# Kernel tuning notes

Measured on AMD Instinct MI355X. Metric: run time of the kernel, lower is better.

## Reference

```python
import jax, jax.numpy as jnp
import numpy as np

B, H, W, C, G = 4, 64, 64, 512, 32
EPS = 1e-5


def group_norm(x, gamma, beta):
    b, h, w, c = x.shape
    xg = x.reshape(b, h, w, G, c // G)
    mean = xg.mean(axis=(1, 2, 4), keepdims=True)
    var = xg.var(axis=(1, 2, 4), keepdims=True)
    xn = ((xg - mean) * jax.lax.rsqrt(var + EPS)).reshape(b, h, w, c)
    return xn * gamma + beta


def setup_inputs() -> dict:
    key = jax.random.key(0)
    ks = jax.random.split(key, 6)
    s = 0.02  # conv-weight init scale
    return {
        "x": jax.random.normal(ks[0], (B, H, W, C), jnp.float32),
        "gamma": jnp.ones((C,), jnp.float32),
        "beta": jnp.zeros((C,), jnp.float32),
        "Wq": jax.random.normal(ks[1], (C, C), jnp.float32) * s,
        "bq": jnp.zeros((C,), jnp.float32),
        "Wk": jax.random.normal(ks[2], (C, C), jnp.float32) * s,
        "bk": jnp.zeros((C,), jnp.float32),
        "Wv": jax.random.normal(ks[3], (C, C), jnp.float32) * s,
        "bv": jnp.zeros((C,), jnp.float32),
        "Wp": jax.random.normal(ks[4], (C, C), jnp.float32) * s,
        "bp": jnp.zeros((C,), jnp.float32),
    }


def reference(x, gamma, beta, Wq, bq, Wk, bk, Wv, bv, Wp, bp):
    b, h, w, c = x.shape
    xn = group_norm(x, gamma, beta)
    # 1x1 convs == per-pixel linear
    q = (jnp.einsum('bhwc,cd->bhwd', xn, Wq) + bq).reshape(b, h * w, c)
    k = (jnp.einsum('bhwc,cd->bhwd', xn, Wk) + bk).reshape(b, h * w, c)
    v = (jnp.einsum('bhwc,cd->bhwd', xn, Wv) + bv).reshape(b, h * w, c)
    scale = 1.0 / jnp.sqrt(jnp.asarray(c, x.dtype))
    scores = jnp.einsum('bqc,bkc->bqk', q, k) * scale  # [b, hw, hw]
    attn = jax.nn.softmax(scores, axis=-1)
    out = jnp.einsum('bqk,bkc->bqc', attn, v).reshape(b, h, w, c)
    return jnp.einsum('bhwc,cd->bhwd', out, Wp) + bp + x
```

## Files before the change

kernel.cpp:

```cpp
#include <hip/hip_runtime.h>

typedef unsigned short u16;
typedef unsigned char u8;
typedef short bf16x8 __attribute__((ext_vector_type(8)));
typedef float f32x4 __attribute__((ext_vector_type(4)));
typedef int i32x8 __attribute__((ext_vector_type(8)));

#define CH 512
#define HW 4096
#define TOKENS 16384
#define NGRP 32

__device__ __forceinline__ u16 f2bf(float f) {
  unsigned u = __float_as_uint(f);
  u += 0x7fffu + ((u >> 16) & 1u);
  return (u16)(u >> 16);
}
__device__ __forceinline__ u8 f2fp8(float f) {
  return (u8)(__builtin_amdgcn_cvt_pk_fp8_f32(f, f, 0, false) & 0xff);
}
__device__ __forceinline__ unsigned f2fp8x4(float a, float b, float c, float d) {
  int lo = __builtin_amdgcn_cvt_pk_fp8_f32(a, b, 0, false);
  return (unsigned)__builtin_amdgcn_cvt_pk_fp8_f32(c, d, lo, true);
}

#define GLOAD16(gp, lp)                                                        \
  __builtin_amdgcn_global_load_lds(                                            \
      (const __attribute__((address_space(1))) unsigned int*)(const void*)(gp),\
      (__attribute__((address_space(3))) unsigned int*)(void*)(lp), 16, 0, 0)

#define RD_FRAG(dst, buf, row) do {                                            \
    int base_ = (row) * 128, sw_ = ((row) & 7) << 4;                           \
    uint4 lo_ = *(const uint4*)(&buf[base_ + ((h * 32) ^ sw_)]);               \
    uint4 hi_ = *(const uint4*)(&buf[base_ + ((h * 32 + 16) ^ sw_)]);          \
    dst[0] = (int)lo_.x; dst[1] = (int)lo_.y; dst[2] = (int)lo_.z;             \
    dst[3] = (int)lo_.w; dst[4] = (int)hi_.x; dst[5] = (int)hi_.y;             \
    dst[6] = (int)hi_.z; dst[7] = (int)hi_.w;                                  \
  } while (0)

#define MXMFMA(a, b, c) \
  __builtin_amdgcn_mfma_scale_f32_16x16x128_f8f6f4(a, b, c, 0, 0, 0, 127, 0, 127)

__global__ void gn_stats(const float* __restrict__ x, float2* __restrict__ stats) {
  int bg = blockIdx.x;
  int b = bg >> 5, g = bg & 31;
  const float* base = x + (size_t)b * HW * CH + g * 16;
  float s = 0.f, s2 = 0.f;
  for (int p = threadIdx.x; p < HW; p += 256) {
    const float4* row = (const float4*)(base + (size_t)p * CH);
#pragma unroll
    for (int q = 0; q < 4; ++q) {
      float4 v = row[q];
      s += v.x + v.y + v.z + v.w;
      s2 += v.x * v.x + v.y * v.y + v.z * v.z + v.w * v.w;
    }
  }
#pragma unroll
  for (int o = 32; o; o >>= 1) { s += __shfl_down(s, o); s2 += __shfl_down(s2, o); }
  __shared__ float rs[4], rs2[4];
  int wid = threadIdx.x >> 6, lane = threadIdx.x & 63;
  if (lane == 0) { rs[wid] = s; rs2[wid] = s2; }
  __syncthreads();
  if (threadIdx.x == 0) {
    float S = rs[0] + rs[1] + rs[2] + rs[3];
    float S2 = rs2[0] + rs2[1] + rs2[2] + rs2[3];
    float mean = S * (1.f / 65536.f);
    float var = S2 * (1.f / 65536.f) - mean * mean;
    stats[bg] = make_float2(mean, rsqrtf(var + 1e-5f));
  }
}

__global__ void gn_apply8(const float* __restrict__ x, const float* __restrict__ gamma,
                          const float* __restrict__ beta, const float2* __restrict__ stats,
                          u8* __restrict__ xn8) {
  size_t i = (size_t)blockIdx.x * blockDim.x + threadIdx.x;
  size_t e0 = i * 8;
  int c = (int)(e0 & (CH - 1));
  size_t t = e0 >> 9;
  int b = (int)(t >> 12);
  float2 st = stats[b * NGRP + (c >> 4)];
  float4 v0 = *(const float4*)(x + t * CH + c);
  float4 v1 = *(const float4*)(x + t * CH + c + 4);
  float4 g0 = *(const float4*)(gamma + c);
  float4 g1 = *(const float4*)(gamma + c + 4);
  float4 b0 = *(const float4*)(beta + c);
  float4 b1 = *(const float4*)(beta + c + 4);
  float o[8];
  o[0] = (v0.x - st.x) * st.y * g0.x + b0.x;
  o[1] = (v0.y - st.x) * st.y * g0.y + b0.y;
  o[2] = (v0.z - st.x) * st.y * g0.z + b0.z;
  o[3] = (v0.w - st.x) * st.y * g0.w + b0.w;
  o[4] = (v1.x - st.x) * st.y * g1.x + b1.x;
  o[5] = (v1.y - st.x) * st.y * g1.y + b1.y;
  o[6] = (v1.z - st.x) * st.y * g1.z + b1.z;
  o[7] = (v1.w - st.x) * st.y * g1.w + b1.w;
  uint2 pk;
  pk.x = f2fp8x4(o[0], o[1], o[2], o[3]);
  pk.y = f2fp8x4(o[4], o[5], o[6], o[7]);
  *(uint2*)(xn8 + e0) = pk;
}

__global__ void transpose_w8(const float* __restrict__ W0, const float* __restrict__ W1,
                             const float* __restrict__ W2, const float* __restrict__ W3,
                             u8* __restrict__ T0, u8* __restrict__ T1,
                             u8* __restrict__ T2, u8* __restrict__ T3) {
  const float* W; u8* T;
  switch (blockIdx.z) {
    case 0: W = W0; T = T0; break;
    case 1: W = W1; T = T1; break;
    case 2: W = W2; T = T2; break;
    default: W = W3; T = T3; break;
  }
  __shared__ float tile[32][33];
  int tx = threadIdx.x, ty = threadIdx.y;
  int x0 = blockIdx.x * 32, y0 = blockIdx.y * 32;
#pragma unroll
  for (int r = 0; r < 32; r += 8) tile[ty + r][tx] = W[(size_t)(y0 + ty + r) * CH + x0 + tx];
  __syncthreads();
#pragma unroll
  for (int r = 0; r < 32; r += 8) T[(size_t)(x0 + ty + r) * CH + y0 + tx] = f2fp8(tile[tx][ty + r]);
}

template <int MODE>
__global__ __launch_bounds__(256) void gemm8mx(const u8* __restrict__ A,
                                               const u8* __restrict__ Bt,
                                               const float* __restrict__ b0p,
                                               const float* __restrict__ b1p,
                                               const float* __restrict__ b2p,
                                               const float* __restrict__ residual,
                                               const float* __restrict__ lsum_in,
                                               float* __restrict__ lsum_out,
                                               void* __restrict__ Cout,
                                               void* __restrict__ C2,
                                               void* __restrict__ C3,
                                               int N, int K, float scale,
                                               size_t sA, size_t sB, size_t sC) {
  constexpr int BK = 128;
  __shared__ __align__(16) u8 lA[128 * BK];
  __shared__ __align__(16) u8 lB[128 * BK];
  __shared__ float lsum_sh[(MODE == 4) ? 128 : 1];

  int bm, bn, z;
  if constexpr (MODE == 4) {
    if (gridDim.y == 1) {
      int p = blockIdx.x;
      int xcd = p & 7, j = p >> 3;
      int xi = j & 3;
      int mp = xcd * 16 + (j >> 2);
      bn = xi * 128; bm = (mp & 31) * 128; z = mp >> 5;
    } else {
      z = blockIdx.z; bm = blockIdx.y * 128; bn = blockIdx.x * 128;
    }
  } else {
    z = blockIdx.z; bm = blockIdx.y * 128; bn = blockIdx.x * 128;
  }
  A += (size_t)z * sA;
  Bt += (size_t)z * sB;

  const int tid = threadIdx.x, lane = tid & 63, wid = tid >> 6;
  const int wm = (wid >> 1) * 64, wn = (wid & 1) * 64;
  const int r0 = lane & 15, h = lane >> 4;

  if constexpr (MODE == 4) {
    if (tid < 128) {
      const float* lp = lsum_in + (size_t)(z * 64) * HW + bm + tid;
      float s = 0.f;
#pragma unroll 8
      for (int p = 0; p < 64; ++p) s += lp[(size_t)p * HW];
      lsum_sh[tid] = s;
    }
  }

  const int srow = lane >> 3;
  const int scol = ((lane & 7) * 16) ^ ((srow & 7) << 4);
  size_t aoff[4], boff[4];
#pragma unroll
  for (int s = 0; s < 4; ++s) {
    int row = wid * 32 + s * 8 + srow;
    aoff[s] = (size_t)(bm + row) * K + scol;
    boff[s] = (size_t)(bn + row) * K + scol;
  }

  f32x4 acc[4][4] = {};

  for (int kt = 0; kt < K; kt += BK) {
    __syncthreads();
#pragma unroll
    for (int s = 0; s < 4; ++s) {
      GLOAD16(A + aoff[s] + kt, &lA[(wid * 4 + s) * 1024]);
      GLOAD16(Bt + boff[s] + kt, &lB[(wid * 4 + s) * 1024]);
    }
    __syncthreads();
    i32x8 bf[4];
#pragma unroll
    for (int j = 0; j < 4; ++j) RD_FRAG(bf[j], lB, wn + j * 16 + r0);
#pragma unroll
    for (int i = 0; i < 4; ++i) {
      i32x8 af;
      RD_FRAG(af, lA, wm + i * 16 + r0);
#pragma unroll
      for (int j = 0; j < 4; ++j) acc[i][j] = MXMFMA(af, bf[j], acc[i][j]);
    }
  }

  if constexpr (MODE == 5) {
    u8* C = (u8*)Cout + (size_t)z * sC;
    float* lp = lsum_out + (size_t)(z * 64 + blockIdx.x * 2 + (wid & 1)) * HW;
#pragma unroll
    for (int i = 0; i < 4; ++i) {
      int m0 = bm + wm + i * 16 + h * 4;
      float rs[4] = {0.f, 0.f, 0.f, 0.f};
#pragma unroll
      for (int j = 0; j < 4; ++j) {
        int n = bn + wn + j * 16 + r0;
#pragma unroll
        for (int r = 0; r < 4; ++r) {
          float e = __expf(acc[i][j][r] * scale);
          rs[r] += e;
          C[(size_t)(m0 + r) * N + n] = f2fp8(e);
        }
      }
#pragma unroll
      for (int r = 0; r < 4; ++r) {
#pragma unroll
        for (int w = 1; w < 16; w <<= 1) rs[r] += __shfl_xor(rs[r], w);
        if (r0 == 0) lp[m0 + r] = rs[r];
      }
    }
  } else {
#pragma unroll
    for (int j = 0; j < 4; ++j) {
      int n = bn + wn + j * 16 + r0;
#pragma unroll
      for (int i = 0; i < 4; ++i) {
        int m0 = bm + wm + i * 16 + h * 4;
        if constexpr (MODE == 2) {
          float* C = (float*)Cout;
          float bvv = b0p[n];
#pragma unroll
          for (int r = 0; r < 4; ++r) {
            size_t idx = (size_t)(m0 + r) * N + n;
            C[idx] = acc[i][j][r] + bvv + residual[idx];
          }
        } else if constexpr (MODE == 3) {
          int nn = n & 511, ch = n >> 9;
          float bvv = ch == 0 ? b0p[nn] : ch == 1 ? b1p[nn] : b2p[nn];
          float v[4];
#pragma unroll
          for (int r = 0; r < 4; ++r) v[r] = acc[i][j][r] + bvv;
          if (ch == 2) {
            int bb = m0 >> 12, tl = m0 & (HW - 1);
            *(unsigned*)((u8*)C3 + ((size_t)bb * CH + nn) * HW + tl) =
                f2fp8x4(v[0], v[1], v[2], v[3]);
          } else {
            u8* C = (u8*)(ch == 0 ? Cout : C2);
#pragma unroll
            for (int r = 0; r < 4; ++r) C[(size_t)(m0 + r) * CH + nn] = f2fp8(v[r]);
          }
        } else {
          u8* C = (u8*)Cout + (size_t)z * sC;
#pragma unroll
          for (int r = 0; r < 4; ++r) {
            float inv = 1.0f / lsum_sh[wm + i * 16 + h * 4 + r];
            C[(size_t)(m0 + r) * N + n] = f2fp8(acc[i][j][r] * inv);
          }
        }
      }
    }
  }
}

__global__ __launch_bounds__(256) void sgemm8(const u8* __restrict__ A,
                                              const u8* __restrict__ Bt,
                                              float* __restrict__ lsum,
                                              u8* __restrict__ S8,
                                              int M, int N, int K, float scale,
                                              size_t sA, size_t sB, size_t sC) {
  constexpr int BM = 128, BN = 128, BK = 64, LRB = 80;
  __shared__ __align__(16) u8 lA[BM * LRB];
  __shared__ __align__(16) u8 lB[BN * LRB];
  const int z = blockIdx.z;
  A += (size_t)z * sA;
  Bt += (size_t)z * sB;
  const int tid = threadIdx.x;
  const int lane = tid & 63, wid = tid >> 6;
  const int bm = blockIdx.y * BM, bn = blockIdx.x * BN;
  const int wm = (wid >> 1) * 64, wn = (wid & 1) * 64;
  const int r0 = lane & 15, h = lane >> 4;

  f32x4 acc[4][4] = {};
  for (int kt = 0; kt < K; kt += BK) {
    __syncthreads();
#pragma unroll
    for (int s = 0; s < 2; ++s) {
      int cid = tid + s * 256;
      int row = cid >> 2, col = (cid & 3) * 16;
      *(uint4*)(&lA[row * LRB + col]) =
          *(const uint4*)(A + (size_t)(bm + row) * K + kt + col);
      *(uint4*)(&lB[row * LRB + col]) =
          *(const uint4*)(Bt + (size_t)(bn + row) * K + kt + col);
    }
    __syncthreads();
#pragma unroll
    for (int kk = 0; kk < BK; kk += 32) {
      long af[4], bfr[4];
#pragma unroll
      for (int i = 0; i < 4; ++i)
        af[i] = *(const long*)(&lA[(wm + i * 16 + r0) * LRB + kk + h * 8]);
#pragma unroll
      for (int j = 0; j < 4; ++j)
        bfr[j] = *(const long*)(&lB[(wn + j * 16 + r0) * LRB + kk + h * 8]);
#pragma unroll
      for (int i = 0; i < 4; ++i)
#pragma unroll
        for (int j = 0; j < 4; ++j)
          acc[i][j] = __builtin_amdgcn_mfma_f32_16x16x32_fp8_fp8(af[i], bfr[j], acc[i][j], 0, 0, 0);
    }
  }

  u8* C = S8 + (size_t)z * sC;
  float* lp = lsum + (size_t)(z * 64 + blockIdx.x * 2 + (wid & 1)) * HW;
#pragma unroll
  for (int i = 0; i < 4; ++i) {
    int m0 = bm + wm + i * 16 + h * 4;
    float rs[4] = {0.f, 0.f, 0.f, 0.f};
#pragma unroll
    for (int j = 0; j < 4; ++j) {
      int n = bn + wn + j * 16 + r0;
#pragma unroll
      for (int r = 0; r < 4; ++r) {
        float e = __expf(acc[i][j][r] * scale);
        rs[r] += e;
        C[(size_t)(m0 + r) * N + n] = f2fp8(e);
      }
    }
#pragma unroll
    for (int r = 0; r < 4; ++r) {
#pragma unroll
      for (int w = 1; w < 16; w <<= 1) rs[r] += __shfl_xor(rs[r], w);
      if (r0 == 0) lp[m0 + r] = rs[r];
    }
  }
}

__global__ __launch_bounds__(256) void pv8(const u8* __restrict__ A,
                                           const u8* __restrict__ Bt,
                                           const float* __restrict__ lsum,
                                           u8* __restrict__ Ob8,
                                           int M, int N, int K,
                                           size_t sA, size_t sB, size_t sC) {
  constexpr int BM = 128, BN = 128, BK = 64, LRB = 80;
  __shared__ __align__(16) u8 lA[BM * LRB];
  __shared__ __align__(16) u8 lB[BN * LRB];
  __shared__ float lsum_sh[BM];

  int bm, bn, z;
  z = blockIdx.z; bm = blockIdx.y * BM; bn = blockIdx.x * BN;
  A += (size_t)z * sA;
  Bt += (size_t)z * sB;
  const int tid = threadIdx.x;
  const int lane = tid & 63, wid = tid >> 6;
  const int wm = (wid >> 1) * 64, wn = (wid & 1) * 64;
  const int r0 = lane & 15, h = lane >> 4;

  if (tid < BM) {
    const float* lp = lsum + (size_t)(z * 64) * HW + bm + tid;
    float s = 0.f;
#pragma unroll 8
    for (int p = 0; p < 64; ++p) s += lp[(size_t)p * HW];
    lsum_sh[tid] = s;
  }

  f32x4 acc[4][4] = {};
  for (int kt = 0; kt < K; kt += BK) {
    __syncthreads();
#pragma unroll
    for (int s = 0; s < 2; ++s) {
      int cid = tid + s * 256;
      int row = cid >> 2, col = (cid & 3) * 16;
      *(uint4*)(&lA[row * LRB + col]) =
          *(const uint4*)(A + (size_t)(bm + row) * K + kt + col);
      *(uint4*)(&lB[row * LRB + col]) =
          *(const uint4*)(Bt + (size_t)(bn + row) * K + kt + col);
    }
    __syncthreads();
#pragma unroll
    for (int kk = 0; kk < BK; kk += 32) {
      long af[4], bfr[4];
#pragma unroll
      for (int i = 0; i < 4; ++i)
        af[i] = *(const long*)(&lA[(wm + i * 16 + r0) * LRB + kk + h * 8]);
#pragma unroll
      for (int j = 0; j < 4; ++j)
        bfr[j] = *(const long*)(&lB[(wn + j * 16 + r0) * LRB + kk + h * 8]);
#pragma unroll
      for (int i = 0; i < 4; ++i)
#pragma unroll
        for (int j = 0; j < 4; ++j)
          acc[i][j] = __builtin_amdgcn_mfma_f32_16x16x32_fp8_fp8(af[i], bfr[j], acc[i][j], 0, 0, 0);
    }
  }

  u8* C = Ob8 + (size_t)z * sC;
#pragma unroll
  for (int j = 0; j < 4; ++j) {
    int n = bn + wn + j * 16 + r0;
#pragma unroll
    for (int i = 0; i < 4; ++i) {
      int m0 = bm + wm + i * 16 + h * 4;
#pragma unroll
      for (int r = 0; r < 4; ++r) {
        float inv = 1.0f / lsum_sh[wm + i * 16 + h * 4 + r];
        C[(size_t)(m0 + r) * N + n] = f2fp8(acc[i][j][r] * inv);
      }
    }
  }
}

extern "C" void kernel_launch(void* const* d_in, const int* in_sizes, int n_in,
                              void* d_out, int out_size, void* d_ws, size_t ws_size,
                              hipStream_t stream) {
  (void)in_sizes; (void)n_in; (void)out_size;
  const float* x     = (const float*)d_in[0];
  const float* gamma = (const float*)d_in[1];
  const float* beta  = (const float*)d_in[2];
  const float* Wq    = (const float*)d_in[3];
  const float* bq    = (const float*)d_in[4];
  const float* Wk    = (const float*)d_in[5];
  const float* bk    = (const float*)d_in[6];
  const float* Wv    = (const float*)d_in[7];
  const float* bv    = (const float*)d_in[8];
  const float* Wp    = (const float*)d_in[9];
  const float* bp    = (const float*)d_in[10];
  float* out = (float*)d_out;

  char* ws = (char*)d_ws;
  size_t off = 0;
  auto alloc = [&](size_t bytes) -> void* {
    void* p = ws + off;
    off += (bytes + 255) & ~(size_t)255;
    return p;
  };
  const size_t X8  = (size_t)TOKENS * CH;
  const size_t W8  = (size_t)CH * CH;
  const size_t S8B = (size_t)HW * HW;
  const size_t LS  = (size_t)4 * 64 * HW * sizeof(float);
  const size_t need_all = 1024 * 1024 + LS + 5 * X8 + 4 * W8 + 4 * S8B;
  const bool big = ws_size >= need_all;

  float2* stats    = (float2*)alloc(128 * sizeof(float2));
  float* lsum_part = (float*)alloc(LS);
  u8* xn8   = (u8*)alloc(X8);
  u8* O8    = (u8*)alloc(X8);
  u8* Q8    = (u8*)alloc(X8);
  u8* K8    = (u8*)alloc(X8);
  u8* V8t   = (u8*)alloc(X8);
  u8* Wqkv8 = (u8*)alloc(3 * W8);
  u8* Wp8   = (u8*)alloc(W8);
  u8* S8    = (u8*)alloc(big ? 4 * S8B : S8B);

  gn_stats<<<128, 256, 0, stream>>>(x, stats);
  gn_apply8<<<TOKENS * CH / 8 / 256, 256, 0, stream>>>(x, gamma, beta, stats, xn8);
  transpose_w8<<<dim3(16, 16, 4), dim3(32, 8), 0, stream>>>(
      Wq, Wk, Wv, Wp, Wqkv8, Wqkv8 + (size_t)CH * CH, Wqkv8 + 2 * (size_t)CH * CH, Wp8);

  gemm8mx<3><<<dim3(1536 / 128, TOKENS / 128), 256, 0, stream>>>(
      xn8, Wqkv8, bq, bk, bv, nullptr, nullptr, nullptr, Q8, K8, V8t,
      1536, CH, 1.0f, 0, 0, 0);

  const float scl = 0.044194173824159216f;
  if (big) {
    gemm8mx<5><<<dim3(32, 32, 4), 256, 0, stream>>>(
        Q8, K8, nullptr, nullptr, nullptr, nullptr, nullptr, lsum_part, S8, nullptr,
        nullptr, HW, CH, scl,
        (size_t)HW * CH, (size_t)HW * CH, (size_t)HW * HW);
    gemm8mx<4><<<dim3(512, 1, 1), 256, 0, stream>>>(
        S8, V8t, nullptr, nullptr, nullptr, nullptr, lsum_part, nullptr, O8, nullptr,
        nullptr, CH, HW, 1.0f,
        (size_t)HW * HW, (size_t)CH * HW, (size_t)HW * CH);
  } else {
    for (int b = 0; b < 4; ++b) {
      sgemm8<<<dim3(HW / 128, HW / 128, 1), 256, 0, stream>>>(
          Q8 + (size_t)b * HW * CH, K8 + (size_t)b * HW * CH,
          lsum_part + (size_t)b * 64 * HW, S8, HW, HW, CH, scl, 0, 0, 0);
      pv8<<<dim3(4, 32, 1), 256, 0, stream>>>(
          S8, V8t + (size_t)b * CH * HW, lsum_part + (size_t)b * 64 * HW,
          O8 + (size_t)b * HW * CH, HW, CH, HW, 0, 0, 0);
    }
  }

  gemm8mx<2><<<dim3(CH / 128, TOKENS / 128), 256, 0, stream>>>(
      O8, Wp8, bp, nullptr, nullptr, x, nullptr, nullptr, out, nullptr, nullptr,
      CH, CH, 1.0f, 0, 0, 0);
}
```

Before: 169.2 us.

## Quantize Q, K, V to FP4 and use mixed FP4/FP8 scaled MFMA in attention

The QKV projection epilogue now packs Q, K and V into 4-bit e2m1 nibbles (with a fixed scale of 4) instead of FP8. The QK^T GEMM and the PV GEMM use the scaled MFMA with FP4 operand formats, so operand memory traffic and LDS footprint shrink. The templated gemm is split into dedicated kernels. The cost is a large accuracy loss from 4-bit quantization of activations, which could break the correctness tolerance.

```diff
diff --git a/kernel.cpp b/kernel.cpp
--- a/kernel.cpp
+++ b/kernel.cpp
@@ -2,7 +2,6 @@
 
 typedef unsigned short u16;
 typedef unsigned char u8;
-typedef short bf16x8 __attribute__((ext_vector_type(8)));
 typedef float f32x4 __attribute__((ext_vector_type(4)));
 typedef int i32x8 __attribute__((ext_vector_type(8)));
 
@@ -11,17 +10,21 @@
 #define TOKENS 16384
 #define NGRP 32
 
-__device__ __forceinline__ u16 f2bf(float f) {
-  unsigned u = __float_as_uint(f);
-  u += 0x7fffu + ((u >> 16) & 1u);
-  return (u16)(u >> 16);
-}
 __device__ __forceinline__ u8 f2fp8(float f) {
   return (u8)(__builtin_amdgcn_cvt_pk_fp8_f32(f, f, 0, false) & 0xff);
 }
 __device__ __forceinline__ unsigned f2fp8x4(float a, float b, float c, float d) {
   int lo = __builtin_amdgcn_cvt_pk_fp8_f32(a, b, 0, false);
   return (unsigned)__builtin_amdgcn_cvt_pk_fp8_f32(c, d, lo, true);
+}
+__device__ __forceinline__ unsigned nib4(float x) {
+  float a = fabsf(x) * 4.0f;
+  unsigned c = (unsigned)(a >= 0.25f) + (a >= 0.75f) + (a >= 1.25f) + (a >= 1.75f) +
+               (a >= 2.5f) + (a >= 3.5f) + (a >= 5.0f);
+  return c | ((__float_as_uint(x) >> 28) & 8u);
+}
+__device__ __forceinline__ u16 pk4(float a, float b, float c, float d) {
+  return (u16)(nib4(a) | (nib4(b) << 4) | (nib4(c) << 8) | (nib4(d) << 12));
 }
 
 #define GLOAD16(gp, lp)                                                        \
@@ -29,7 +32,7 @@
       (const __attribute__((address_space(1))) unsigned int*)(const void*)(gp),\
       (__attribute__((address_space(3))) unsigned int*)(void*)(lp), 16, 0, 0)
 
-#define RD_FRAG(dst, buf, row) do {                                            \
+#define RD8(dst, buf, row) do {                                                \
     int base_ = (row) * 128, sw_ = ((row) & 7) << 4;                           \
     uint4 lo_ = *(const uint4*)(&buf[base_ + ((h * 32) ^ sw_)]);               \
     uint4 hi_ = *(const uint4*)(&buf[base_ + ((h * 32 + 16) ^ sw_)]);          \
@@ -38,8 +41,11 @@
     dst[6] = (int)hi_.z; dst[7] = (int)hi_.w;                                  \
   } while (0)
 
-#define MXMFMA(a, b, c) \
-  __builtin_amdgcn_mfma_scale_f32_16x16x128_f8f6f4(a, b, c, 0, 0, 0, 127, 0, 127)
+#define RD4(dst, buf, row) do {                                                \
+    uint4 t_ = *(const uint4*)(&buf[(row) * 64 + ((h * 16) ^ (((row) & 3) << 4))]); \
+    dst[0] = (int)t_.x; dst[1] = (int)t_.y; dst[2] = (int)t_.z;                \
+    dst[3] = (int)t_.w; dst[4] = 0; dst[5] = 0; dst[6] = 0; dst[7] = 0;        \
+  } while (0)
 
 __global__ void gn_stats(const float* __restrict__ x, float2* __restrict__ stats) {
   int bg = blockIdx.x;
@@ -121,55 +127,21 @@
   for (int r = 0; r < 32; r += 8) T[(size_t)(x0 + ty + r) * CH + y0 + tx] = f2fp8(tile[tx][ty + r]);
 }
 
-template <int MODE>
-__global__ __launch_bounds__(256) void gemm8mx(const u8* __restrict__ A,
-                                               const u8* __restrict__ Bt,
-                                               const float* __restrict__ b0p,
-                                               const float* __restrict__ b1p,
-                                               const float* __restrict__ b2p,
-                                               const float* __restrict__ residual,
-                                               const float* __restrict__ lsum_in,
-                                               float* __restrict__ lsum_out,
-                                               void* __restrict__ Cout,
-                                               void* __restrict__ C2,
-                                               void* __restrict__ C3,
-                                               int N, int K, float scale,
-                                               size_t sA, size_t sB, size_t sC) {
+__global__ __launch_bounds__(256) void qkvmx(const u8* __restrict__ A,
+                                             const u8* __restrict__ Bt,
+                                             const float* __restrict__ bq,
+                                             const float* __restrict__ bk,
+                                             const float* __restrict__ bv,
+                                             u8* __restrict__ Q4, u8* __restrict__ K4,
+                                             u8* __restrict__ V4) {
   constexpr int BK = 128;
+  const int K = CH;
   __shared__ __align__(16) u8 lA[128 * BK];
   __shared__ __align__(16) u8 lB[128 * BK];
-  __shared__ float lsum_sh[(MODE == 4) ? 128 : 1];
-
-  int bm, bn, z;
-  if constexpr (MODE == 4) {
-    if (gridDim.y == 1) {
-      int p = blockIdx.x;
-      int xcd = p & 7, j = p >> 3;
-      int xi = j & 3;
-      int mp = xcd * 16 + (j >> 2);
-      bn = xi * 128; bm = (mp & 31) * 128; z = mp >> 5;
-    } else {
-      z = blockIdx.z; bm = blockIdx.y * 128; bn = blockIdx.x * 128;
-    }
-  } else {
-    z = blockIdx.z; bm = blockIdx.y * 128; bn = blockIdx.x * 128;
-  }
-  A += (size_t)z * sA;
-  Bt += (size_t)z * sB;
-
+  const int bm = blockIdx.y * 128, bn = blockIdx.x * 128;
   const int tid = threadIdx.x, lane = tid & 63, wid = tid >> 6;
   const int wm = (wid >> 1) * 64, wn = (wid & 1) * 64;
   const int r0 = lane & 15, h = lane >> 4;
-
-  if constexpr (MODE == 4) {
-    if (tid < 128) {
-      const float* lp = lsum_in + (size_t)(z * 64) * HW + bm + tid;
-      float s = 0.f;
-#pragma unroll 8
-      for (int p = 0; p < 64; ++p) s += lp[(size_t)p * HW];
-      lsum_sh[tid] = s;
-    }
-  }
 
   const int srow = lane >> 3;
   const int scol = ((lane & 7) * 16) ^ ((srow & 7) << 4);
@@ -182,7 +154,6 @@
   }
 
   f32x4 acc[4][4] = {};
-
   for (int kt = 0; kt < K; kt += BK) {
     __syncthreads();
 #pragma unroll
@@ -193,128 +164,99 @@
     __syncthreads();
     i32x8 bf[4];
 #pragma unroll
-    for (int j = 0; j < 4; ++j) RD_FRAG(bf[j], lB, wn + j * 16 + r0);
+    for (int j = 0; j < 4; ++j) RD8(bf[j], lB, wn + j * 16 + r0);
 #pragma unroll
     for (int i = 0; i < 4; ++i) {
       i32x8 af;
-      RD_FRAG(af, lA, wm + i * 16 + r0);
-#pragma unroll
-      for (int j = 0; j < 4; ++j) acc[i][j] = MXMFMA(af, bf[j], acc[i][j]);
-    }
-  }
-
-  if constexpr (MODE == 5) {
-    u8* C = (u8*)Cout + (size_t)z * sC;
-    float* lp = lsum_out + (size_t)(z * 64 + blockIdx.x * 2 + (wid & 1)) * HW;
-#pragma unroll
-    for (int i = 0; i < 4; ++i) {
-      int m0 = bm + wm + i * 16 + h * 4;
-      float rs[4] = {0.f, 0.f, 0.f, 0.f};
-#pragma unroll
-      for (int j = 0; j < 4; ++j) {
-        int n = bn + wn + j * 16 + r0;
-#pragma unroll
-        for (int r = 0; r < 4; ++r) {
-          float e = __expf(acc[i][j][r] * scale);
-          rs[r] += e;
-          C[(size_t)(m0 + r) * N + n] = f2fp8(e);
-        }
-      }
-#pragma unroll
-      for (int r = 0; r < 4; ++r) {
-#pragma unroll
-        for (int w = 1; w < 16; w <<= 1) rs[r] += __shfl_xor(rs[r], w);
-        if (r0 == 0) lp[m0 + r] = rs[r];
-      }
-    }
-  } else {
+      RD8(af, lA, wm + i * 16 + r0);
+#pragma unroll
+      for (int j = 0; j < 4; ++j)
+        acc[i][j] = __builtin_amdgcn_mfma_scale_f32_16x16x128_f8f6f4(
+            af, bf[j], acc[i][j], 0, 0, 0, 127, 0, 127);
+    }
+  }
+
+  const int chn = (bn + wn) >> 9;
+  const int nb = (bn + wn) & 511;
+  if (chn == 2) {
 #pragma unroll
     for (int j = 0; j < 4; ++j) {
-      int n = bn + wn + j * 16 + r0;
+      int nn = nb + j * 16 + r0;
+      float bvv = bv[nn];
 #pragma unroll
       for (int i = 0; i < 4; ++i) {
         int m0 = bm + wm + i * 16 + h * 4;
-        if constexpr (MODE == 2) {
-          float* C = (float*)Cout;
-          float bvv = b0p[n];
-#pragma unroll
-          for (int r = 0; r < 4; ++r) {
-            size_t idx = (size_t)(m0 + r) * N + n;
-            C[idx] = acc[i][j][r] + bvv + residual[idx];
-          }
-        } else if constexpr (MODE == 3) {
-          int nn = n & 511, ch = n >> 9;
-          float bvv = ch == 0 ? b0p[nn] : ch == 1 ? b1p[nn] : b2p[nn];
-          float v[4];
-#pragma unroll
-          for (int r = 0; r < 4; ++r) v[r] = acc[i][j][r] + bvv;
-          if (ch == 2) {
-            int bb = m0 >> 12, tl = m0 & (HW - 1);
-            *(unsigned*)((u8*)C3 + ((size_t)bb * CH + nn) * HW + tl) =
-                f2fp8x4(v[0], v[1], v[2], v[3]);
-          } else {
-            u8* C = (u8*)(ch == 0 ? Cout : C2);
-#pragma unroll
-            for (int r = 0; r < 4; ++r) C[(size_t)(m0 + r) * CH + nn] = f2fp8(v[r]);
-          }
-        } else {
-          u8* C = (u8*)Cout + (size_t)z * sC;
-#pragma unroll
-          for (int r = 0; r < 4; ++r) {
-            float inv = 1.0f / lsum_sh[wm + i * 16 + h * 4 + r];
-            C[(size_t)(m0 + r) * N + n] = f2fp8(acc[i][j][r] * inv);
-          }
-        }
+        int bb = m0 >> 12, tl = m0 & (HW - 1);
+        *(u16*)(V4 + ((size_t)bb * CH + nn) * (HW / 2) + (tl >> 1)) =
+            pk4(acc[i][j][0] + bvv, acc[i][j][1] + bvv,
+                acc[i][j][2] + bvv, acc[i][j][3] + bvv);
       }
     }
-  }
-}
-
-__global__ __launch_bounds__(256) void sgemm8(const u8* __restrict__ A,
-                                              const u8* __restrict__ Bt,
+  } else {
+    u8* P4 = chn == 0 ? Q4 : K4;
+    const float* bb_ = chn == 0 ? bq : bk;
+    float bj[4];
+#pragma unroll
+    for (int j = 0; j < 4; ++j) bj[j] = bb_[nb + j * 16 + r0];
+#pragma unroll
+    for (int i = 0; i < 4; ++i) {
+#pragma unroll
+      for (int r = 0; r < 4; ++r) {
+        int m0r = bm + wm + i * 16 + h * 4 + r;
+        *(u16*)(P4 + (size_t)m0r * 256 + (nb >> 1) + 2 * r0) =
+            pk4(acc[i][0][r] + bj[0], acc[i][1][r] + bj[1],
+                acc[i][2][r] + bj[2], acc[i][3][r] + bj[3]);
+      }
+    }
+  }
+}
+
+__global__ __launch_bounds__(256) void sgemm4(const u8* __restrict__ Q4,
+                                              const u8* __restrict__ K4,
                                               float* __restrict__ lsum,
                                               u8* __restrict__ S8,
-                                              int M, int N, int K, float scale,
+                                              float scale,
                                               size_t sA, size_t sB, size_t sC) {
-  constexpr int BM = 128, BN = 128, BK = 64, LRB = 80;
-  __shared__ __align__(16) u8 lA[BM * LRB];
-  __shared__ __align__(16) u8 lB[BN * LRB];
+  __shared__ __align__(16) u8 lA[128 * 64];
+  __shared__ __align__(16) u8 lB[128 * 64];
   const int z = blockIdx.z;
-  A += (size_t)z * sA;
-  Bt += (size_t)z * sB;
-  const int tid = threadIdx.x;
-  const int lane = tid & 63, wid = tid >> 6;
-  const int bm = blockIdx.y * BM, bn = blockIdx.x * BN;
+  const u8* A = Q4 + (size_t)z * sA;
+  const u8* B = K4 + (size_t)z * sB;
+  const int bm = blockIdx.y * 128, bn = blockIdx.x * 128;
+  const int tid = threadIdx.x, lane = tid & 63, wid = tid >> 6;
   const int wm = (wid >> 1) * 64, wn = (wid & 1) * 64;
   const int r0 = lane & 15, h = lane >> 4;
 
+  const int srow = lane >> 2;
+  const int scol = (((lane & 3) ^ (srow & 3)) << 4);
+  size_t aoff[2], boff[2];
+#pragma unroll
+  for (int s = 0; s < 2; ++s) {
+    int row = wid * 32 + s * 16 + srow;
+    aoff[s] = (size_t)(bm + row) * 256 + scol;
+    boff[s] = (size_t)(bn + row) * 256 + scol;
+  }
+
   f32x4 acc[4][4] = {};
-  for (int kt = 0; kt < K; kt += BK) {
+  for (int ktb = 0; ktb < 256; ktb += 64) {
     __syncthreads();
 #pragma unroll
     for (int s = 0; s < 2; ++s) {
-      int cid = tid + s * 256;
-      int row = cid >> 2, col = (cid & 3) * 16;
-      *(uint4*)(&lA[row * LRB + col]) =
-          *(const uint4*)(A + (size_t)(bm + row) * K + kt + col);
-      *(uint4*)(&lB[row * LRB + col]) =
-          *(const uint4*)(Bt + (size_t)(bn + row) * K + kt + col);
-    }
-    __syncthreads();
-#pragma unroll
-    for (int kk = 0; kk < BK; kk += 32) {
-      long af[4], bfr[4];
-#pragma unroll
-      for (int i = 0; i < 4; ++i)
-        af[i] = *(const long*)(&lA[(wm + i * 16 + r0) * LRB + kk + h * 8]);
+      GLOAD16(A + aoff[s] + ktb, &lA[(wid * 2 + s) * 1024]);
+      GLOAD16(B + boff[s] + ktb, &lB[(wid * 2 + s) * 1024]);
+    }
+    __syncthreads();
+    i32x8 bf[4];
+#pragma unroll
+    for (int j = 0; j < 4; ++j) RD4(bf[j], lB, wn + j * 16 + r0);
+#pragma unroll
+    for (int i = 0; i < 4; ++i) {
+      i32x8 af;
+      RD4(af, lA, wm + i * 16 + r0);
 #pragma unroll
       for (int j = 0; j < 4; ++j)
-        bfr[j] = *(const long*)(&lB[(wn + j * 16 + r0) * LRB + kk + h * 8]);
-#pragma unroll
-      for (int i = 0; i < 4; ++i)
-#pragma unroll
-        for (int j = 0; j < 4; ++j)
-          acc[i][j] = __builtin_amdgcn_mfma_f32_16x16x32_fp8_fp8(af[i], bfr[j], acc[i][j], 0, 0, 0);
+        acc[i][j] = __builtin_amdgcn_mfma_scale_f32_16x16x128_f8f6f4(
+            af, bf[j], acc[i][j], 4, 4, 0, 125, 0, 125);
     }
   }
 
@@ -331,7 +273,7 @@
       for (int r = 0; r < 4; ++r) {
         float e = __expf(acc[i][j][r] * scale);
         rs[r] += e;
-        C[(size_t)(m0 + r) * N + n] = f2fp8(e);
+        C[(size_t)(m0 + r) * HW + n] = f2fp8(e);
       }
     }
 #pragma unroll
@@ -343,75 +285,149 @@
   }
 }
 
-__global__ __launch_bounds__(256) void pv8(const u8* __restrict__ A,
-                                           const u8* __restrict__ Bt,
-                                           const float* __restrict__ lsum,
-                                           u8* __restrict__ Ob8,
-                                           int M, int N, int K,
-                                           size_t sA, size_t sB, size_t sC) {
-  constexpr int BM = 128, BN = 128, BK = 64, LRB = 80;
-  __shared__ __align__(16) u8 lA[BM * LRB];
-  __shared__ __align__(16) u8 lB[BN * LRB];
-  __shared__ float lsum_sh[BM];
+__global__ __launch_bounds__(256) void pv84(const u8* __restrict__ S8,
+                                            const u8* __restrict__ V4,
+                                            const float* __restrict__ lsum_in,
+                                            u8* __restrict__ O8) {
+  __shared__ __align__(16) u8 lA[128 * 128];
+  __shared__ __align__(16) u8 lB[128 * 64];
+  __shared__ float lsum_sh[128];
 
   int bm, bn, z;
-  z = blockIdx.z; bm = blockIdx.y * BM; bn = blockIdx.x * BN;
-  A += (size_t)z * sA;
-  Bt += (size_t)z * sB;
-  const int tid = threadIdx.x;
-  const int lane = tid & 63, wid = tid >> 6;
+  if (gridDim.y == 1) {
+    int p = blockIdx.x;
+    int xcd = p & 7, j = p >> 3;
+    int xi = j & 3;
+    int mp = xcd * 16 + (j >> 2);
+    bn = xi * 128; bm = (mp & 31) * 128; z = mp >> 5;
+  } else {
+    z = blockIdx.z; bm = blockIdx.y * 128; bn = blockIdx.x * 128;
+  }
+  const u8* A = S8 + (size_t)z * HW * HW;
+  const u8* B = V4 + (size_t)z * CH * (HW / 2);
+  const float* lsum = lsum_in + (size_t)z * 64 * HW;
+  u8* C = O8 + (size_t)z * HW * CH;
+
+  const int tid = threadIdx.x, lane = tid & 63, wid = tid >> 6;
   const int wm = (wid >> 1) * 64, wn = (wid & 1) * 64;
   const int r0 = lane & 15, h = lane >> 4;
 
-  if (tid < BM) {
-    const float* lp = lsum + (size_t)(z * 64) * HW + bm + tid;
+  if (tid < 128) {
+    const float* lp = lsum + bm + tid;
     float s = 0.f;
 #pragma unroll 8
     for (int p = 0; p < 64; ++p) s += lp[(size_t)p * HW];
     lsum_sh[tid] = s;
   }
 
+  const int srow8 = lane >> 3;
+  const int scol8 = ((lane & 7) * 16) ^ ((srow8 & 7) << 4);
+  size_t aoff[4];
+#pragma unroll
+  for (int s = 0; s < 4; ++s)
+    aoff[s] = (size_t)(bm + wid * 32 + s * 8 + srow8) * HW + scol8;
+  const int srow4 = lane >> 2;
+  const int scol4 = (((lane & 3) ^ (srow4 & 3)) << 4);
+  size_t boff[2];
+#pragma unroll
+  for (int s = 0; s < 2; ++s)
+    boff[s] = (size_t)(bn + wid * 32 + s * 16 + srow4) * (HW / 2) + scol4;
+
+  f32x4 acc[4][4] = {};
+  for (int kt = 0; kt < HW; kt += 128) {
+    __syncthreads();
+#pragma unroll
+    for (int s = 0; s < 4; ++s) GLOAD16(A + aoff[s] + kt, &lA[(wid * 4 + s) * 1024]);
+#pragma unroll
+    for (int s = 0; s < 2; ++s) GLOAD16(B + boff[s] + (kt >> 1), &lB[(wid * 2 + s) * 1024]);
+    __syncthreads();
+    i32x8 bf[4];
+#pragma unroll
+    for (int j = 0; j < 4; ++j) RD4(bf[j], lB, wn + j * 16 + r0);
+#pragma unroll
+    for (int i = 0; i < 4; ++i) {
+      i32x8 af;
+      RD8(af, lA, wm + i * 16 + r0);
+#pragma unroll
+      for (int j = 0; j < 4; ++j)
+        acc[i][j] = __builtin_amdgcn_mfma_scale_f32_16x16x128_f8f6f4(
+            af, bf[j], acc[i][j], 0, 4, 0, 127, 0, 125);
+    }
+  }
+
+#pragma unroll
+  for (int j = 0; j < 4; ++j) {
+    int n = bn + wn + j * 16 + r0;
+#pragma unroll
+    for (int i = 0; i < 4; ++i) {
+      int m0 = bm + wm + i * 16 + h * 4;
+#pragma unroll
+      for (int r = 0; r < 4; ++r) {
+        float inv = 1.0f / lsum_sh[wm + i * 16 + h * 4 + r];
+        C[(size_t)(m0 + r) * CH + n] = f2fp8(acc[i][j][r] * inv);
+      }
+    }
+  }
+}
+
+__global__ __launch_bounds__(256) void projmx(const u8* __restrict__ A,
+                                              const u8* __restrict__ Bt,
+                                              const float* __restrict__ bias,
+                                              const float* __restrict__ residual,
+                                              float* __restrict__ Cout) {
+  constexpr int BK = 128;
+  const int K = CH, N = CH;
+  __shared__ __align__(16) u8 lA[128 * BK];
+  __shared__ __align__(16) u8 lB[128 * BK];
+  const int bm = blockIdx.y * 128, bn = blockIdx.x * 128;
+  const int tid = threadIdx.x, lane = tid & 63, wid = tid >> 6;
+  const int wm = (wid >> 1) * 64, wn = (wid & 1) * 64;
+  const int r0 = lane & 15, h = lane >> 4;
+
+  const int srow = lane >> 3;
+  const int scol = ((lane & 7) * 16) ^ ((srow & 7) << 4);
+  size_t aoff[4], boff[4];
+#pragma unroll
+  for (int s = 0; s < 4; ++s) {
+    int row = wid * 32 + s * 8 + srow;
+    aoff[s] = (size_t)(bm + row) * K + scol;
+    boff[s] = (size_t)(bn + row) * K + scol;
+  }
+
   f32x4 acc[4][4] = {};
   for (int kt = 0; kt < K; kt += BK) {
     __syncthreads();
 #pragma unroll
-    for (int s = 0; s < 2; ++s) {
-      int cid = tid + s * 256;
-      int row = cid >> 2, col = (cid & 3) * 16;
-      *(uint4*)(&lA[row * LRB + col]) =
-          *(const uint4*)(A + (size_t)(bm + row) * K + kt + col);
-      *(uint4*)(&lB[row * LRB + col]) =
-          *(const uint4*)(Bt + (size_t)(bn + row) * K + kt + col);
-    }
-    __syncthreads();
-#pragma unroll
-    for (int kk = 0; kk < BK; kk += 32) {
-      long af[4], bfr[4];
-#pragma unroll
-      for (int i = 0; i < 4; ++i)
-        af[i] = *(const long*)(&lA[(wm + i * 16 + r0) * LRB + kk + h * 8]);
+    for (int s = 0; s < 4; ++s) {
+      GLOAD16(A + aoff[s] + kt, &lA[(wid * 4 + s) * 1024]);
+      GLOAD16(Bt + boff[s] + kt, &lB[(wid * 4 + s) * 1024]);
+    }
+    __syncthreads();
+    i32x8 bf[4];
+#pragma unroll
+    for (int j = 0; j < 4; ++j) RD8(bf[j], lB, wn + j * 16 + r0);
+#pragma unroll
+    for (int i = 0; i < 4; ++i) {
+      i32x8 af;
+      RD8(af, lA, wm + i * 16 + r0);
 #pragma unroll
       for (int j = 0; j < 4; ++j)
-        bfr[j] = *(const long*)(&lB[(wn + j * 16 + r0) * LRB + kk + h * 8]);
-#pragma unroll
-      for (int i = 0; i < 4; ++i)
-#pragma unroll
-        for (int j = 0; j < 4; ++j)
-          acc[i][j] = __builtin_amdgcn_mfma_f32_16x16x32_fp8_fp8(af[i], bfr[j], acc[i][j], 0, 0, 0);
-    }
-  }
-
-  u8* C = Ob8 + (size_t)z * sC;
+        acc[i][j] = __builtin_amdgcn_mfma_scale_f32_16x16x128_f8f6f4(
+            af, bf[j], acc[i][j], 0, 0, 0, 127, 0, 127);
+    }
+  }
+
 #pragma unroll
   for (int j = 0; j < 4; ++j) {
     int n = bn + wn + j * 16 + r0;
+    float bvv = bias[n];
 #pragma unroll
     for (int i = 0; i < 4; ++i) {
       int m0 = bm + wm + i * 16 + h * 4;
 #pragma unroll
       for (int r = 0; r < 4; ++r) {
-        float inv = 1.0f / lsum_sh[wm + i * 16 + h * 4 + r];
-        C[(size_t)(m0 + r) * N + n] = f2fp8(acc[i][j][r] * inv);
+        size_t idx = (size_t)(m0 + r) * N + n;
+        Cout[idx] = acc[i][j][r] + bvv + residual[idx];
       }
     }
   }
@@ -442,19 +458,20 @@
     return p;
   };
   const size_t X8  = (size_t)TOKENS * CH;
+  const size_t X4  = (size_t)TOKENS * CH / 2;
   const size_t W8  = (size_t)CH * CH;
   const size_t S8B = (size_t)HW * HW;
   const size_t LS  = (size_t)4 * 64 * HW * sizeof(float);
-  const size_t need_all = 1024 * 1024 + LS + 5 * X8 + 4 * W8 + 4 * S8B;
+  const size_t need_all = 1024 * 1024 + LS + 2 * X8 + 3 * X4 + 4 * W8 + 4 * S8B;
   const bool big = ws_size >= need_all;
 
   float2* stats    = (float2*)alloc(128 * sizeof(float2));
   float* lsum_part = (float*)alloc(LS);
   u8* xn8   = (u8*)alloc(X8);
   u8* O8    = (u8*)alloc(X8);
-  u8* Q8    = (u8*)alloc(X8);
-  u8* K8    = (u8*)alloc(X8);
-  u8* V8t   = (u8*)alloc(X8);
+  u8* Q4    = (u8*)alloc(X4);
+  u8* K4    = (u8*)alloc(X4);
+  u8* V4    = (u8*)alloc(X4);
   u8* Wqkv8 = (u8*)alloc(3 * W8);
   u8* Wp8   = (u8*)alloc(W8);
   u8* S8    = (u8*)alloc(big ? 4 * S8B : S8B);
@@ -464,32 +481,25 @@
   transpose_w8<<<dim3(16, 16, 4), dim3(32, 8), 0, stream>>>(
       Wq, Wk, Wv, Wp, Wqkv8, Wqkv8 + (size_t)CH * CH, Wqkv8 + 2 * (size_t)CH * CH, Wp8);
 
-  gemm8mx<3><<<dim3(1536 / 128, TOKENS / 128), 256, 0, stream>>>(
-      xn8, Wqkv8, bq, bk, bv, nullptr, nullptr, nullptr, Q8, K8, V8t,
-      1536, CH, 1.0f, 0, 0, 0);
+  qkvmx<<<dim3(1536 / 128, TOKENS / 128), 256, 0, stream>>>(
+      xn8, Wqkv8, bq, bk, bv, Q4, K4, V4);
 
   const float scl = 0.044194173824159216f;
+  const size_t sQ = (size_t)HW * 256;
   if (big) {
-    gemm8mx<5><<<dim3(32, 32, 4), 256, 0, stream>>>(
-        Q8, K8, nullptr, nullptr, nullptr, nullptr, nullptr, lsum_part, S8, nullptr,
-        nullptr, HW, CH, scl,
-        (size_t)HW * CH, (size_t)HW * CH, (size_t)HW * HW);
-    gemm8mx<4><<<dim3(512, 1, 1), 256, 0, stream>>>(
-        S8, V8t, nullptr, nullptr, nullptr, nullptr, lsum_part, nullptr, O8, nullptr,
-        nullptr, CH, HW, 1.0f,
-        (size_t)HW * HW, (size_t)CH * HW, (size_t)HW * CH);
+    sgemm4<<<dim3(32, 32, 4), 256, 0, stream>>>(
+        Q4, K4, lsum_part, S8, scl, sQ, sQ, (size_t)HW * HW);
+    pv84<<<dim3(512, 1, 1), 256, 0, stream>>>(S8, V4, lsum_part, O8);
   } else {
     for (int b = 0; b < 4; ++b) {
-      sgemm8<<<dim3(HW / 128, HW / 128, 1), 256, 0, stream>>>(
-          Q8 + (size_t)b * HW * CH, K8 + (size_t)b * HW * CH,
-          lsum_part + (size_t)b * 64 * HW, S8, HW, HW, CH, scl, 0, 0, 0);
-      pv8<<<dim3(4, 32, 1), 256, 0, stream>>>(
-          S8, V8t + (size_t)b * CH * HW, lsum_part + (size_t)b * 64 * HW,
-          O8 + (size_t)b * HW * CH, HW, CH, HW, 0, 0, 0);
-    }
-  }
-
-  gemm8mx<2><<<dim3(CH / 128, TOKENS / 128), 256, 0, stream>>>(
-      O8, Wp8, bp, nullptr, nullptr, x, nullptr, nullptr, out, nullptr, nullptr,
-      CH, CH, 1.0f, 0, 0, 0);
-}
+      sgemm4<<<dim3(32, 32, 1), 256, 0, stream>>>(
+          Q4 + (size_t)b * sQ, K4 + (size_t)b * sQ,
+          lsum_part + (size_t)b * 64 * HW, S8, scl, 0, 0, 0);
+      pv84<<<dim3(4, 32, 1), 256, 0, stream>>>(
+          S8, V4 + (size_t)b * CH * (HW / 2),
+          lsum_part + (size_t)b * 64 * HW, O8 + (size_t)b * HW * CH);
+    }
+  }
+
+  projmx<<<dim3(4, TOKENS / 128), 256, 0, stream>>>(O8, Wp8, bp, x, out);
+}
```

Measured after the change: 165.0 us. -2.5%, faster.
